# Performance work log

Measured on AMD Instinct MI355X. Metric: run time of the kernel, lower is better.

Reference implementation:

```python
import jax, jax.numpy as jnp
import numpy as np

CONF_THRESHOLD = 0.7

def setup_inputs() -> dict:
    key = jax.random.key(0)
    ks = jax.random.split(key, 8)
    B, T, D, H, GH = 16384, 48, 32, 1024, 128
    s = lambda fan: 1.0 / np.sqrt(fan)
    return {
        "x":   jax.random.normal(ks[0], (B, T, D), jnp.float32),
        "gW1": jax.random.normal(ks[1], (D, GH), jnp.float32) * s(D),
        "gb1": jnp.zeros((GH,), jnp.float32),
        "gW2": jax.random.normal(ks[2], (GH, 2), jnp.float32) * s(GH),
        "gb2": jnp.zeros((2,), jnp.float32),
        "nW1": jax.random.normal(ks[3], (T * D, H), jnp.float32) * s(T * D),
        "nb1": jnp.zeros((H,), jnp.float32),
        "nW2": jax.random.normal(ks[4], (H, 2), jnp.float32) * s(H),
        "nb2": jnp.zeros((2,), jnp.float32),
        "aW1": jax.random.normal(ks[5], (T * D, H), jnp.float32) * s(T * D),
        "ab1": jnp.zeros((H,), jnp.float32),
        "aW2": jax.random.normal(ks[6], (H, 2), jnp.float32) * s(H),
        "ab2": jnp.zeros((2,), jnp.float32),
    }

def _gate(x, gW1, gb1, gW2, gb2):
    # mean-pool over time, 2-layer MLP, softmax -> [B, 2] class probs
    h = jax.nn.relu(jnp.mean(x, axis=1) @ gW1 + gb1)
    return jax.nn.softmax(h @ gW2 + gb2, axis=-1)

def _expert(x_flat, W1, b1, W2, b2):
    return jax.nn.relu(x_flat @ W1 + b1) @ W2 + b2

def reference(x, gW1, gb1, gW2, gb2, nW1, nb1, nW2, nb2, aW1, ab1, aW2, ab2):
    B = x.shape[0]
    gate_outputs = _gate(x, gW1, gb1, gW2, gb2)          # [B, 2]
    gate_probs = jnp.max(gate_outputs, axis=1)           # [B]
    gate_decisions = jnp.argmax(gate_outputs, axis=1)    # [B] in {0,1}

    # adaptive routing: low-confidence samples fall back to the normal expert
    high_conf = gate_probs >= CONF_THRESHOLD
    abnormal_mask = high_conf & (gate_decisions == 1)
    # normal_mask = (high_conf & dec==0) | ~high_conf  == ~abnormal_mask (partition)

    x_flat = x.reshape(B, -1)
    normal_out = _expert(x_flat, nW1, nb1, nW2, nb2)     # [B, 2]
    abnormal_out = _expert(x_flat, aW1, ab1, aW2, ab2)   # [B, 2]
    outputs = jnp.where(abnormal_mask[:, None], abnormal_out, normal_out)
    return outputs, gate_decisions, gate_probs
```

## Files before the change

kernel.cpp:

```cpp
#include <hip/hip_runtime.h>

#define TDIM 48
#define DDIM 32
#define KDIM 1536
#define HDIM 1024
#define GHID 128

typedef unsigned short u16;
typedef __bf16 bf16x8 __attribute__((ext_vector_type(8)));
typedef float  f32x4  __attribute__((ext_vector_type(4)));

typedef const void __attribute__((address_space(1))) gvoid;
typedef void       __attribute__((address_space(3))) lvoid;

__device__ __forceinline__ void gld_lds16(const void* g, void* l) {
    __builtin_amdgcn_global_load_lds((gvoid*)g, (lvoid*)l, 16, 0, 0);
}

__device__ __forceinline__ u16 f2bf(float f) {
    union { float f; unsigned u; } v; v.f = f;
    return (u16)((v.u + 0x7fffu + ((v.u >> 16) & 1u)) >> 16);
}

__global__ __launch_bounds__(64) void gate_kernel(
    const float* __restrict__ x,
    const float* __restrict__ gW1, const float* __restrict__ gb1,
    const float* __restrict__ gW2, const float* __restrict__ gb2,
    u16* __restrict__ Xbf, int* __restrict__ route,
    float* __restrict__ outDec, float* __restrict__ outProb)
{
    const int b    = blockIdx.x;
    const int lane = threadIdx.x;
    const float* xr = x + (size_t)b * KDIM;
    u16* xo = Xbf + (size_t)b * KDIM;

    double a0 = 0, a1 = 0, a2 = 0, a3 = 0;
#pragma unroll
    for (int i = 0; i < 6; ++i) {
        const int idx = i * 256 + lane * 4;
        float4 v = *(const float4*)(xr + idx);
        ushort4 o;
        o.x = f2bf(v.x); o.y = f2bf(v.y); o.z = f2bf(v.z); o.w = f2bf(v.w);
        *(ushort4*)(xo + idx) = o;
        a0 += v.x; a1 += v.y; a2 += v.z; a3 += v.w;
    }
#pragma unroll
    for (int m = 8; m <= 32; m <<= 1) {
        a0 += __shfl_xor(a0, m); a1 += __shfl_xor(a1, m);
        a2 += __shfl_xor(a2, m); a3 += __shfl_xor(a3, m);
    }
    __shared__ double xm[DDIM];
    if (lane < 8) {
        xm[4 * lane + 0] = a0 / 48.0; xm[4 * lane + 1] = a1 / 48.0;
        xm[4 * lane + 2] = a2 / 48.0; xm[4 * lane + 3] = a3 / 48.0;
    }
    __syncthreads();

    double h0 = (double)gb1[lane], h1 = (double)gb1[lane + 64];
#pragma unroll
    for (int d = 0; d < DDIM; ++d) {
        const double xv = xm[d];
        h0 += xv * (double)gW1[d * GHID + lane];
        h1 += xv * (double)gW1[d * GHID + 64 + lane];
    }
    h0 = h0 > 0.0 ? h0 : 0.0;
    h1 = h1 > 0.0 ? h1 : 0.0;
    double z0 = h0 * (double)gW2[lane * 2 + 0] + h1 * (double)gW2[(lane + 64) * 2 + 0];
    double z1 = h0 * (double)gW2[lane * 2 + 1] + h1 * (double)gW2[(lane + 64) * 2 + 1];
#pragma unroll
    for (int m = 1; m <= 32; m <<= 1) {
        z0 += __shfl_xor(z0, m);
        z1 += __shfl_xor(z1, m);
    }
    if (lane == 0) {
        z0 += (double)gb2[0]; z1 += (double)gb2[1];
        const int dec = (z1 > z0) ? 1 : 0;
        const double mz = z0 > z1 ? z0 : z1;
        const double e0 = exp(z0 - mz), e1 = exp(z1 - mz);
        const double p = (e0 > e1 ? e0 : e1) / (e0 + e1);
        const float pf = (float)p;
        outDec[b]  = (float)dec;
        outProb[b] = pf;
        const int high = ((double)pf >= 0.7) ? 1 : 0;
        route[b] = (high && dec) ? 1 : 0;
    }
}

__global__ __launch_bounds__(256) void transpose_cast(
    const float* __restrict__ nW1, const float* __restrict__ aW1,
    u16* __restrict__ W1t)
{
    __shared__ float tile[32][33];
    const int e  = blockIdx.z;
    const float* W = e ? aW1 : nW1;
    u16* Wt = W1t + (size_t)e * HDIM * KDIM;
    const int bx = blockIdx.x;
    const int by = blockIdx.y;
    const int tx = threadIdx.x;
    const int ty = threadIdx.y;
#pragma unroll
    for (int r = 0; r < 32; r += 8)
        tile[ty + r][tx] = W[(size_t)(by * 32 + ty + r) * HDIM + bx * 32 + tx];
    __syncthreads();
#pragma unroll
    for (int r = 0; r < 32; r += 8)
        Wt[(size_t)(bx * 32 + ty + r) * KDIM + by * 32 + tx] = f2bf(tile[tx][ty + r]);
}

__global__ __launch_bounds__(256) void compact_kernel(
    const int* __restrict__ route, int* __restrict__ perm, int* __restrict__ cnt,
    int Bn)
{
    const int b    = blockIdx.x * 256 + threadIdx.x;
    const int lane = threadIdx.x & 63;
    const int active = (b < Bn);
    const int e = active ? route[b] : 0;
    const unsigned long long m1 = __ballot(active && e == 1);
    const unsigned long long m0 = __ballot(active && e == 0);
    const unsigned long long below = (lane == 63) ? ~0ull >> 1 : ((1ull << lane) - 1);
    int base0 = 0, base1 = 0;
    if (lane == 0) {
        if (m0) base0 = atomicAdd(&cnt[0], (int)__popcll(m0));
        if (m1) base1 = atomicAdd(&cnt[1], (int)__popcll(m1));
    }
    base0 = __shfl(base0, 0);
    base1 = __shfl(base1, 0);
    if (active) {
        const int pos = e ? base1 + (int)__popcll(m1 & below)
                          : base0 + (int)__popcll(m0 & below);
        perm[e * Bn + pos] = b;
    }
}

__global__ __launch_bounds__(256, 2) void expert_gemm(
    const u16* __restrict__ Xbf, const u16* __restrict__ W1t,
    const float* __restrict__ nb1, const float* __restrict__ nW2,
    const float* __restrict__ nb2,
    const float* __restrict__ ab1, const float* __restrict__ aW2,
    const float* __restrict__ ab2,
    const int* __restrict__ perm, const int* __restrict__ cnt,
    float* __restrict__ out, int Bn, int mBlocks)
{
    __shared__ __align__(16) u16 Alds[128 * 32];
    __shared__ __align__(16) u16 Blds[128 * 32];
    __shared__ int   permLds[128];
    __shared__ float w2Lds[128 * 2];
    __shared__ float b1Lds[128];

    const int tid = threadIdx.x;
    const int e  = (int)blockIdx.y >= mBlocks;
    const int mb = (int)blockIdx.y - (e ? mBlocks : 0);
    const int cntE = cnt[e];
    const int start = mb * 128;
    if (start >= cntE) return;
    const int valid = min(128, cntE - start);

    const int n0 = (int)blockIdx.x * 128;
    const u16*  W1e = W1t + (size_t)e * HDIM * KDIM;
    const float* b1 = e ? ab1 : nb1;
    const float* w2 = e ? aW2 : nW2;
    const float* b2 = e ? ab2 : nb2;

    if (tid < 128) permLds[tid] = perm[e * Bn + min(start + tid, cntE - 1)];
    if (tid >= 128) {
        const int j = tid - 128;
        b1Lds[j]        = b1[n0 + j];
        w2Lds[j * 2 + 0] = w2[(n0 + j) * 2 + 0];
        w2Lds[j * 2 + 1] = w2[(n0 + j) * 2 + 1];
    }
    __syncthreads();

    const int rA0 = permLds[tid >> 2];
    const int rA1 = permLds[(tid + 256) >> 2];
    const u16* gA0 = Xbf + (size_t)rA0 * KDIM + (tid & 3) * 8;
    const u16* gA1 = Xbf + (size_t)rA1 * KDIM + (tid & 3) * 8;
    const u16* gB0 = W1e + (size_t)(n0 + (tid >> 2)) * KDIM + (tid & 3) * 8;
    const u16* gB1 = W1e + (size_t)(n0 + 64 + (tid >> 2)) * KDIM + (tid & 3) * 8;

    const int wave = tid >> 6;
    const int lane = tid & 63;
    const int wm   = (wave & 1) * 64;
    const int wn   = (wave >> 1) * 64;
    const int l15  = lane & 15;
    const int quad = lane >> 4;

    f32x4 acc[4][4];
#pragma unroll
    for (int i = 0; i < 4; ++i)
#pragma unroll
        for (int j = 0; j < 4; ++j) acc[i][j] = (f32x4)0.f;

    for (int k0 = 0; k0 < KDIM; k0 += 32) {
        gld_lds16(gA0 + k0, &Alds[tid * 8]);
        gld_lds16(gA1 + k0, &Alds[(tid + 256) * 8]);
        gld_lds16(gB0 + k0, &Blds[tid * 8]);
        gld_lds16(gB1 + k0, &Blds[(tid + 256) * 8]);
        __syncthreads();

        bf16x8 af[4], bfv[4];
#pragma unroll
        for (int mi = 0; mi < 4; ++mi)
            af[mi] = *reinterpret_cast<const bf16x8*>(&Alds[(wm + mi * 16 + l15) * 32 + quad * 8]);
#pragma unroll
        for (int ni = 0; ni < 4; ++ni)
            bfv[ni] = *reinterpret_cast<const bf16x8*>(&Blds[(wn + ni * 16 + l15) * 32 + quad * 8]);
#pragma unroll
        for (int mi = 0; mi < 4; ++mi)
#pragma unroll
            for (int ni = 0; ni < 4; ++ni)
                acc[mi][ni] = __builtin_amdgcn_mfma_f32_16x16x32_bf16(af[mi], bfv[ni], acc[mi][ni], 0, 0, 0);
        __syncthreads();
    }

    const float b2_0 = (n0 == 0) ? b2[0] : 0.f;
    const float b2_1 = (n0 == 0) ? b2[1] : 0.f;
#pragma unroll
    for (int mi = 0; mi < 4; ++mi) {
        float p0[4] = {0.f, 0.f, 0.f, 0.f};
        float p1[4] = {0.f, 0.f, 0.f, 0.f};
#pragma unroll
        for (int ni = 0; ni < 4; ++ni) {
            const int col = wn + ni * 16 + l15;
            const float w20 = w2Lds[col * 2 + 0];
            const float w21 = w2Lds[col * 2 + 1];
            const float bb  = b1Lds[col];
#pragma unroll
            for (int r = 0; r < 4; ++r) {
                float h = acc[mi][ni][r] + bb;
                h = fmaxf(h, 0.f);
                p0[r] += h * w20;
                p1[r] += h * w21;
            }
        }
#pragma unroll
        for (int m = 1; m <= 8; m <<= 1) {
#pragma unroll
            for (int r = 0; r < 4; ++r) {
                p0[r] += __shfl_xor(p0[r], m);
                p1[r] += __shfl_xor(p1[r], m);
            }
        }
        if (l15 < 4) {
            const int r = l15;
            const int lrow = wm + mi * 16 + quad * 4 + r;
            if (lrow < valid) {
                const int srow = permLds[lrow];
                atomicAdd(&out[srow * 2 + 0], p0[r] + b2_0);
                atomicAdd(&out[srow * 2 + 1], p1[r] + b2_1);
            }
        }
    }
}

extern "C" void kernel_launch(void* const* d_in, const int* in_sizes, int n_in,
                              void* d_out, int out_size, void* d_ws, size_t ws_size,
                              hipStream_t stream) {
    const float* x   = (const float*)d_in[0];
    const float* gW1 = (const float*)d_in[1];
    const float* gb1 = (const float*)d_in[2];
    const float* gW2 = (const float*)d_in[3];
    const float* gb2 = (const float*)d_in[4];
    const float* nW1 = (const float*)d_in[5];
    const float* nb1 = (const float*)d_in[6];
    const float* nW2 = (const float*)d_in[7];
    const float* nb2 = (const float*)d_in[8];
    const float* aW1 = (const float*)d_in[9];
    const float* ab1 = (const float*)d_in[10];
    const float* aW2 = (const float*)d_in[11];
    const float* ab2 = (const float*)d_in[12];

    float* out = (float*)d_out;
    const int Bn = in_sizes[0] / KDIM;

    char* ws = (char*)d_ws;
    size_t off = 0;
    u16* Xbf = (u16*)(ws + off); off += (size_t)Bn * KDIM * sizeof(u16);
    u16* W1t = (u16*)(ws + off); off += (size_t)2 * HDIM * KDIM * sizeof(u16);
    int* perm = (int*)(ws + off); off += (size_t)2 * Bn * sizeof(int);
    int* cnt  = (int*)(ws + off); off += 2 * sizeof(int);
    int* route = (int*)(ws + off); off += (size_t)Bn * sizeof(int);

    hipMemsetAsync(out, 0, (size_t)2 * Bn * sizeof(float), stream);
    hipMemsetAsync(cnt, 0, 2 * sizeof(int), stream);

    gate_kernel<<<Bn, 64, 0, stream>>>(x, gW1, gb1, gW2, gb2,
                                       Xbf, route, out + 2 * Bn, out + 3 * Bn);

    transpose_cast<<<dim3(HDIM / 32, KDIM / 32, 2), dim3(32, 8), 0, stream>>>(nW1, aW1, W1t);

    compact_kernel<<<(Bn + 255) / 256, 256, 0, stream>>>(route, perm, cnt, Bn);

    const int mBlocks = (Bn + 127) / 128;
    expert_gemm<<<dim3(HDIM / 128, 2 * mBlocks), 256, 0, stream>>>(
        Xbf, W1t, nb1, nW2, nb2, ab1, aW2, ab2, perm, cnt, out, Bn, mBlocks);
}
```

Measured before the change: 272.5 us.

## Fold memsets into gate kernel, pack 4 rows per block, swizzle GEMM grid

```diff
diff --git a/kernel.cpp b/kernel.cpp
--- a/kernel.cpp
+++ b/kernel.cpp
@@ -22,15 +22,18 @@
     return (u16)((v.u + 0x7fffu + ((v.u >> 16) & 1u)) >> 16);
 }
 
-__global__ __launch_bounds__(64) void gate_kernel(
+__global__ __launch_bounds__(256) void gate_kernel(
     const float* __restrict__ x,
     const float* __restrict__ gW1, const float* __restrict__ gb1,
     const float* __restrict__ gW2, const float* __restrict__ gb2,
-    u16* __restrict__ Xbf, int* __restrict__ route,
-    float* __restrict__ outDec, float* __restrict__ outProb)
+    u16* __restrict__ Xbf, int* __restrict__ route, int* __restrict__ cnt,
+    float* __restrict__ out, float* __restrict__ outDec, float* __restrict__ outProb)
 {
-    const int b    = blockIdx.x;
-    const int lane = threadIdx.x;
+    const int wave = threadIdx.x >> 6;
+    const int lane = threadIdx.x & 63;
+    const int b    = blockIdx.x * 4 + wave;
+    if (blockIdx.x == 0 && threadIdx.x < 2) cnt[threadIdx.x] = 0;
+
     const float* xr = x + (size_t)b * KDIM;
     u16* xo = Xbf + (size_t)b * KDIM;
 
@@ -49,17 +52,19 @@
         a0 += __shfl_xor(a0, m); a1 += __shfl_xor(a1, m);
         a2 += __shfl_xor(a2, m); a3 += __shfl_xor(a3, m);
     }
-    __shared__ double xm[DDIM];
+    __shared__ double xm[4][DDIM];
     if (lane < 8) {
-        xm[4 * lane + 0] = a0 / 48.0; xm[4 * lane + 1] = a1 / 48.0;
-        xm[4 * lane + 2] = a2 / 48.0; xm[4 * lane + 3] = a3 / 48.0;
-    }
-    __syncthreads();
+        xm[wave][4 * lane + 0] = a0 / 48.0; xm[wave][4 * lane + 1] = a1 / 48.0;
+        xm[wave][4 * lane + 2] = a2 / 48.0; xm[wave][4 * lane + 3] = a3 / 48.0;
+    }
+    __builtin_amdgcn_wave_barrier();
+    __builtin_amdgcn_s_waitcnt(0);
+    __threadfence_block();
 
     double h0 = (double)gb1[lane], h1 = (double)gb1[lane + 64];
 #pragma unroll
     for (int d = 0; d < DDIM; ++d) {
-        const double xv = xm[d];
+        const double xv = xm[wave][d];
         h0 += xv * (double)gW1[d * GHID + lane];
         h1 += xv * (double)gW1[d * GHID + 64 + lane];
     }
@@ -81,6 +86,8 @@
         const float pf = (float)p;
         outDec[b]  = (float)dec;
         outProb[b] = pf;
+        out[2 * b + 0] = 0.f;
+        out[2 * b + 1] = 0.f;
         const int high = ((double)pf >= 0.7) ? 1 : 0;
         route[b] = (high && dec) ? 1 : 0;
     }
@@ -148,14 +155,18 @@
     __shared__ float b1Lds[128];
 
     const int tid = threadIdx.x;
-    const int e  = (int)blockIdx.y >= mBlocks;
-    const int mb = (int)blockIdx.y - (e ? mBlocks : 0);
+    const int f    = (int)blockIdx.x;
+    const int g    = f >> 6;
+    const int nIdx = (f >> 3) & 7;
+    const int mGlb = g * 8 + (f & 7);
+    const int e  = mGlb >= mBlocks;
+    const int mb = mGlb - (e ? mBlocks : 0);
     const int cntE = cnt[e];
     const int start = mb * 128;
     if (start >= cntE) return;
     const int valid = min(128, cntE - start);
 
-    const int n0 = (int)blockIdx.x * 128;
+    const int n0 = nIdx * 128;
     const u16*  W1e = W1t + (size_t)e * HDIM * KDIM;
     const float* b1 = e ? ab1 : nb1;
     const float* w2 = e ? aW2 : nW2;
@@ -280,17 +291,15 @@
     int* cnt  = (int*)(ws + off); off += 2 * sizeof(int);
     int* route = (int*)(ws + off); off += (size_t)Bn * sizeof(int);
 
-    hipMemsetAsync(out, 0, (size_t)2 * Bn * sizeof(float), stream);
-    hipMemsetAsync(cnt, 0, 2 * sizeof(int), stream);
-
-    gate_kernel<<<Bn, 64, 0, stream>>>(x, gW1, gb1, gW2, gb2,
-                                       Xbf, route, out + 2 * Bn, out + 3 * Bn);
+    gate_kernel<<<Bn / 4, 256, 0, stream>>>(x, gW1, gb1, gW2, gb2,
+                                            Xbf, route, cnt,
+                                            out, out + 2 * Bn, out + 3 * Bn);
 
     transpose_cast<<<dim3(HDIM / 32, KDIM / 32, 2), dim3(32, 8), 0, stream>>>(nW1, aW1, W1t);
 
     compact_kernel<<<(Bn + 255) / 256, 256, 0, stream>>>(route, perm, cnt, Bn);
 
     const int mBlocks = (Bn + 127) / 128;
-    expert_gemm<<<dim3(HDIM / 128, 2 * mBlocks), 256, 0, stream>>>(
+    expert_gemm<<<8 * 2 * mBlocks, 256, 0, stream>>>(
         Xbf, W1t, nb1, nW2, nb2, ab1, aW2, ab2, perm, cnt, out, Bn, mBlocks);
 }
```

New measurement: 253.8 us. 1.07x faster.
